# Optimization experiments

Measured on AMD Instinct MI355X. Metric: run time of the kernel, lower is better.

## Reference

```python
import jax, jax.numpy as jnp
import numpy as np

B, L_IMG, L_TXT, DM, H, D = 1, 4096, 512, 3072, 24, 128
EPS = 1e-6


def _rms(x, scale):
    # flax nnx RMSNorm: x * rsqrt(mean(x^2) + eps) * scale
    var = jnp.mean(jnp.square(x), axis=-1, keepdims=True)
    return x * jax.lax.rsqrt(var + EPS) * scale


def _qkv(x, W, qn, kn):
    b, l = x.shape[:2]
    qkv = (x @ W).reshape(b, l, 3, H, D).transpose(2, 0, 3, 1, 4)  # [3,B,H,L,D]
    q, k, v = qkv[0], qkv[1], qkv[2]
    return _rms(q, qn), _rms(k, kn), v


def setup_inputs() -> dict:
    key = jax.random.key(0)
    ks = jax.random.split(key, 8)
    s = 0.02
    return {
        "hidden_states": jax.random.normal(ks[0], (B, L_IMG, DM), jnp.float32),
        "encoder_hidden_states": jax.random.normal(ks[1], (B, L_TXT, DM), jnp.float32),
        "image_rotary_emb": jax.random.normal(ks[2], (L_TXT + L_IMG, D // 2, 4), jnp.float32),
        "W_iqkv": jax.random.normal(ks[3], (DM, 3 * H * D), jnp.float32) * s,
        "W_eqkv": jax.random.normal(ks[4], (DM, 3 * H * D), jnp.float32) * s,
        "W_iproj": jax.random.normal(ks[5], (H * D, DM), jnp.float32) * s,
        "b_iproj": jnp.zeros((DM,), jnp.float32),
        "W_eproj": jax.random.normal(ks[6], (H * D, DM), jnp.float32) * s,
        "b_eproj": jnp.zeros((DM,), jnp.float32),
        "qn_scale": jnp.ones((D,), jnp.float32),
        "kn_scale": jnp.ones((D,), jnp.float32),
        "eqn_scale": jnp.ones((D,), jnp.float32),
        "ekn_scale": jnp.ones((D,), jnp.float32),
    }


def reference(hidden_states, encoder_hidden_states, image_rotary_emb,
              W_iqkv, W_eqkv, W_iproj, b_iproj, W_eproj, b_eproj,
              qn_scale, kn_scale, eqn_scale, ekn_scale):
    scale = D ** -0.5
    l_txt = encoder_hidden_states.shape[1]

    q, k, v = _qkv(hidden_states, W_iqkv, qn_scale, kn_scale)           # [B,H,L_img,D]
    eq, ek, ev = _qkv(encoder_hidden_states, W_eqkv, eqn_scale, ekn_scale)

    q = jnp.concatenate((eq, q), axis=2)   # [B,H,L,D], L = L_txt + L_img
    k = jnp.concatenate((ek, k), axis=2)
    v = jnp.concatenate((ev, v), axis=2)

    # RoPE: freqs_cis [L, D/2, 2, 2]
    fc = image_rotary_emb.reshape(image_rotary_emb.shape[0], image_rotary_emb.shape[1], 2, 2)

    def rope(x):
        x_ = x.reshape(*x.shape[:-1], -1, 1, 2)  # [B,H,L,D/2,1,2]
        out = fc[..., 0] * x_[..., 0] + fc[..., 1] * x_[..., 1]  # [B,H,L,D/2,2]
        return out.reshape(*x.shape).astype(x.dtype)

    q, k = rope(q), rope(k)

    # flatten heads into feature dim BEFORE attention (faithful to original)
    def merge(x):
        b, h, l, d = x.shape
        return x.transpose(0, 2, 1, 3).reshape(b, l, h * d)

    qm, km, vm = merge(q), merge(k), merge(v)  # [B,L,H*D]

    attn = jax.nn.softmax(jnp.einsum('bqd,bkd->bqk', qm, km) * scale, axis=-1)
    out = jnp.einsum('bqk,bkd->bqd', attn, vm)  # [B,L,H*D]

    ctx_out, img_out = out[:, :l_txt], out[:, l_txt:]
    img_out = img_out @ W_iproj + b_iproj
    ctx_out = ctx_out @ W_eproj + b_eproj
    return img_out, ctx_out
```

## Files before the change

kernel.cpp:

```cpp
#include <hip/hip_runtime.h>
#include <hip/hip_bf16.h>
#include <cstdint>

typedef __attribute__((ext_vector_type(8))) short u16x8;
typedef _Float16 f16_t;
typedef __attribute__((ext_vector_type(8))) f16_t f16x8;
typedef __attribute__((ext_vector_type(4))) float f32x4;

#define L_TOT 4608
#define L_TXT 512
#define L_IMG 4096
#define NH 24
#define HD 128
#define DMODEL 3072
#define NQKV 9216
#define LOG2E 1.44269504088896340736f
#define S_SHIFT 32.0f

__device__ __forceinline__ ushort f2h(float f) {
  union { f16_t h; ushort u; } c; c.h = (f16_t)f; return c.u;
}
__device__ __forceinline__ float h2f(ushort u) {
  union { ushort u; f16_t h; } c; c.u = u; return (float)c.h;
}
__device__ __forceinline__ void gload16(const ushort* g, ushort* l) {
  __builtin_amdgcn_global_load_lds((const __attribute__((address_space(1))) void*)g,
                                   (__attribute__((address_space(3))) void*)l, 16, 0, 0);
}

__global__ void cvt_f32_f16(const float* __restrict__ src, ushort* __restrict__ dst,
                            int n8) {
  const int i = blockIdx.x * 256 + threadIdx.x;
  if (i >= n8) return;
  const f32x4 a = *(const f32x4*)(src + (size_t)i * 8);
  const f32x4 b = *(const f32x4*)(src + (size_t)i * 8 + 4);
  alignas(16) ushort o[8];
#pragma unroll
  for (int j = 0; j < 4; ++j) { o[j] = f2h(a[j]); o[4 + j] = f2h(b[j]); }
  *(u16x8*)(dst + (size_t)i * 8) = *(const u16x8*)o;
}

__global__ void tconv_w(const float* __restrict__ src, int C, int c0,
                        ushort* __restrict__ dst) {
  __shared__ ushort tile[64][72];
  const int nb = blockIdx.x << 6, kb = blockIdx.y << 6;
  const int t = threadIdx.x;
  const int lr = t >> 2, lc = (t & 3) << 4;
  const float* sp = src + (size_t)(kb + lr) * C + c0 + nb + lc;
  const f32x4 v0 = *(const f32x4*)sp;
  const f32x4 v1 = *(const f32x4*)(sp + 4);
  const f32x4 v2 = *(const f32x4*)(sp + 8);
  const f32x4 v3 = *(const f32x4*)(sp + 12);
#pragma unroll
  for (int i = 0; i < 4; ++i) {
    tile[lr][lc + i]      = f2h(v0[i]);
    tile[lr][lc + 4 + i]  = f2h(v1[i]);
    tile[lr][lc + 8 + i]  = f2h(v2[i]);
    tile[lr][lc + 12 + i] = f2h(v3[i]);
  }
  __syncthreads();
  const int cl = t & 63, rb = (t >> 6) << 4;
  alignas(16) ushort o[16];
#pragma unroll
  for (int i = 0; i < 16; ++i) o[i] = tile[rb + i][cl];
  ushort* dp = dst + (size_t)(nb + cl) * DMODEL + kb + rb;
  *(u16x8*)dp       = *(const u16x8*)o;
  *(u16x8*)(dp + 8) = *(const u16x8*)(o + 8);
}

__global__ void tconv_h(const ushort* __restrict__ src, ushort* __restrict__ dst,
                        int R, int C) {
  __shared__ ushort tile[64][72];
  const int r0 = blockIdx.y << 6, c0 = blockIdx.x << 6;
  const int t = threadIdx.x;
  const int lr = t >> 2, lc = (t & 3) << 4;
  const ushort* sp = src + (size_t)(r0 + lr) * C + c0 + lc;
  const u16x8 v0 = *(const u16x8*)sp;
  const u16x8 v1 = *(const u16x8*)(sp + 8);
#pragma unroll
  for (int i = 0; i < 8; ++i) {
    tile[lr][lc + i]     = ((const ushort*)&v0)[i];
    tile[lr][lc + 8 + i] = ((const ushort*)&v1)[i];
  }
  __syncthreads();
  const int cl = t & 63, rb = (t >> 6) << 4;
  alignas(16) ushort o[16];
#pragma unroll
  for (int i = 0; i < 16; ++i) o[i] = tile[rb + i][cl];
  ushort* dp = dst + (size_t)(c0 + cl) * R + r0 + rb;
  *(u16x8*)dp       = *(const u16x8*)o;
  *(u16x8*)(dp + 8) = *(const u16x8*)(o + 8);
}

template <int MODE>
__global__ __launch_bounds__(512, 2) void gemm256(
    const ushort* __restrict__ A, int lda, const ushort* __restrict__ Bt, int ldb,
    int M, int N, int K, void* __restrict__ out0, ushort* __restrict__ out1,
    ushort* __restrict__ out2, const float* __restrict__ bias, int l_off, int n_base) {
  __shared__ __align__(16) ushort lds[2][2][2][8192];
  int lin = blockIdx.y * gridDim.x + blockIdx.x;
  {
    const int nwg = gridDim.x * gridDim.y;
    const int q8 = nwg >> 3, r8 = nwg & 7;
    const int xcd = lin & 7, idx = lin >> 3;
    lin = (xcd < r8 ? xcd * (q8 + 1) : r8 * (q8 + 1) + (xcd - r8) * q8) + idx;
  }
  const int m0 = (lin % gridDim.x) << 8, n0 = (lin / gridDim.x) << 8;
  const int tid = threadIdx.x, w = tid >> 6, lane = tid & 63;
  const int wm = w >> 2, wn = w & 3;
  const int lr = lane & 15, g4 = lane >> 4;
  const int srow = lane >> 2;
  const int soff = 8 * ((lane & 3) ^ ((lane >> 3) & 3));
  f32x4 acc[8][4];
#pragma unroll
  for (int a = 0; a < 8; ++a)
#pragma unroll
    for (int b = 0; b < 4; ++b) acc[a][b] = (f32x4){0.f, 0.f, 0.f, 0.f};
  const int nt = K >> 6;

  auto stageA = [&](int h, int kt, int b) {
#pragma unroll
    for (int i = 0; i < 2; ++i) {
      const int j = w * 2 + i;
      gload16(A + (size_t)(m0 + 16 * j + srow) * lda + (kt << 6) + 32 * h + soff,
              &lds[b][h][0][j * 512]);
    }
  };
  auto stageB = [&](int h, int kt, int b) {
#pragma unroll
    for (int i = 0; i < 2; ++i) {
      const int j = w * 2 + i;
      gload16(Bt + (size_t)(n0 + 16 * j + srow) * ldb + (kt << 6) + 32 * h + soff,
              &lds[b][h][1][j * 512]);
    }
  };
  auto readA = [&](int h, int mi, int b) -> f16x8 {
    const int row = wm * 128 + mi * 16 + lr;
    const int byte = row * 64 + ((g4 ^ ((row >> 1) & 3)) << 4);
    return *(const f16x8*)((const char*)&lds[b][h][0][0] + byte);
  };
  auto readB = [&](int h, int ni, int b) -> f16x8 {
    const int row = wn * 64 + ni * 16 + lr;
    const int byte = row * 64 + ((g4 ^ ((row >> 1) & 3)) << 4);
    return *(const f16x8*)((const char*)&lds[b][h][1][0] + byte);
  };

  stageA(0, 0, 0); stageB(0, 0, 0); stageA(1, 0, 0); stageB(1, 0, 0);
  asm volatile("s_waitcnt vmcnt(4)" ::: "memory");
  asm volatile("s_barrier" ::: "memory");

  for (int kt = 0; kt < nt; ++kt) {
    const int c = kt & 1, sb = c ^ 1;
    const int st = (kt + 1 < nt) ? kt + 1 : 0;
    f16x8 bf[4], af[4];
#pragma unroll
    for (int ni = 0; ni < 4; ++ni) bf[ni] = readB(0, ni, c);
#pragma unroll
    for (int m = 0; m < 4; ++m) af[m] = readA(0, m, c);
    stageA(0, st, sb);
    asm volatile("s_barrier" ::: "memory");
    asm volatile("s_waitcnt lgkmcnt(0)" ::: "memory");
    __builtin_amdgcn_sched_barrier(0);
    __builtin_amdgcn_s_setprio(1);
#pragma unroll
    for (int m = 0; m < 4; ++m)
#pragma unroll
      for (int ni = 0; ni < 4; ++ni)
        acc[m][ni] = __builtin_amdgcn_mfma_f32_16x16x32_f16(af[m], bf[ni], acc[m][ni], 0, 0, 0);
    __builtin_amdgcn_s_setprio(0);
    asm volatile("s_barrier" ::: "memory");
#pragma unroll
    for (int m = 0; m < 4; ++m) af[m] = readA(0, 4 + m, c);
    stageB(0, st, sb);
    asm volatile("s_barrier" ::: "memory");
    asm volatile("s_waitcnt lgkmcnt(0)" ::: "memory");
    __builtin_amdgcn_sched_barrier(0);
    __builtin_amdgcn_s_setprio(1);
#pragma unroll
    for (int m = 0; m < 4; ++m)
#pragma unroll
      for (int ni = 0; ni < 4; ++ni)
        acc[4 + m][ni] = __builtin_amdgcn_mfma_f32_16x16x32_f16(af[m], bf[ni], acc[4 + m][ni], 0, 0, 0);
    __builtin_amdgcn_s_setprio(0);
    asm volatile("s_barrier" ::: "memory");
    asm volatile("s_waitcnt vmcnt(4)" ::: "memory");
    asm volatile("s_barrier" ::: "memory");
#pragma unroll
    for (int ni = 0; ni < 4; ++ni) bf[ni] = readB(1, ni, c);
#pragma unroll
    for (int m = 0; m < 4; ++m) af[m] = readA(1, m, c);
    stageA(1, st, sb);
    asm volatile("s_barrier" ::: "memory");
    asm volatile("s_waitcnt lgkmcnt(0)" ::: "memory");
    __builtin_amdgcn_sched_barrier(0);
    __builtin_amdgcn_s_setprio(1);
#pragma unroll
    for (int m = 0; m < 4; ++m)
#pragma unroll
      for (int ni = 0; ni < 4; ++ni)
        acc[m][ni] = __builtin_amdgcn_mfma_f32_16x16x32_f16(af[m], bf[ni], acc[m][ni], 0, 0, 0);
    __builtin_amdgcn_s_setprio(0);
    asm volatile("s_barrier" ::: "memory");
#pragma unroll
    for (int m = 0; m < 4; ++m) af[m] = readA(1, 4 + m, c);
    stageB(1, st, sb);
    asm volatile("s_barrier" ::: "memory");
    asm volatile("s_waitcnt lgkmcnt(0)" ::: "memory");
    __builtin_amdgcn_sched_barrier(0);
    __builtin_amdgcn_s_setprio(1);
#pragma unroll
    for (int m = 0; m < 4; ++m)
#pragma unroll
      for (int ni = 0; ni < 4; ++ni)
        acc[4 + m][ni] = __builtin_amdgcn_mfma_f32_16x16x32_f16(af[m], bf[ni], acc[4 + m][ni], 0, 0, 0);
    __builtin_amdgcn_s_setprio(0);
    asm volatile("s_waitcnt vmcnt(4)" ::: "memory");
    asm volatile("s_barrier" ::: "memory");
  }

  const int rb = (lane >> 4) << 2;
  const int cl = lane & 15;
  if (MODE == 0) {
    const int g = n_base + n0;
    const int which = g / DMODEL;
    const int col0 = g - which * DMODEL;
    ushort* dst = (which == 0) ? (ushort*)out0 : (which == 1) ? out1 : out2;
#pragma unroll
    for (int mi = 0; mi < 8; ++mi)
#pragma unroll
      for (int j = 0; j < 4; ++j) {
        const int l = l_off + m0 + wm * 128 + mi * 16 + rb + j;
        const size_t rbase = (size_t)l * DMODEL + col0 + wn * 64 + cl;
#pragma unroll
        for (int ni = 0; ni < 4; ++ni) dst[rbase + ni * 16] = f2h(acc[mi][ni][j]);
      }
  } else if (MODE == 1) {
    float* outf = (float*)out0;
    float bv[4];
#pragma unroll
    for (int ni = 0; ni < 4; ++ni) bv[ni] = bias[n0 + wn * 64 + ni * 16 + cl];
#pragma unroll
    for (int mi = 0; mi < 8; ++mi)
#pragma unroll
      for (int j = 0; j < 4; ++j) {
        const int r = m0 + wm * 128 + mi * 16 + rb + j;
        const size_t rbase = (size_t)r * N + n0 + wn * 64 + cl;
#pragma unroll
        for (int ni = 0; ni < 4; ++ni) outf[rbase + ni * 16] = acc[mi][ni][j] + bv[ni];
      }
  } else {
    ushort* outb = (ushort*)out0;
    const float sh = (MODE == 3) ? S_SHIFT : 0.0f;
#pragma unroll
    for (int mi = 0; mi < 8; ++mi)
#pragma unroll
      for (int j = 0; j < 4; ++j) {
        const int r = m0 + wm * 128 + mi * 16 + rb + j;
        const size_t rbase = (size_t)r * N + n0 + wn * 64 + cl;
#pragma unroll
        for (int ni = 0; ni < 4; ++ni) outb[rbase + ni * 16] = f2h(acc[mi][ni][j] - sh);
      }
  }
}

template <int MODE>
__global__ void gemm128(const ushort* __restrict__ A, int lda,
                        const ushort* __restrict__ Bt, int ldb,
                        int M, int N, int K, void* __restrict__ out0,
                        ushort* __restrict__ out1, ushort* __restrict__ out2,
                        const float* __restrict__ bias, int l_off, int n_base) {
  __shared__ __align__(16) ushort Alds[128 * 32];
  __shared__ __align__(16) ushort Blds[128 * 32];
  const int m0 = blockIdx.x << 7, n0 = blockIdx.y << 7;
  const int tid = threadIdx.x, wave = tid >> 6, lane = tid & 63;
  const int wr = wave >> 1, wc = wave & 1;
  const int lrow = lane & 15, lk8 = (lane >> 4) << 3;
  f32x4 acc[4][4];
#pragma unroll
  for (int a = 0; a < 4; ++a)
#pragma unroll
    for (int b = 0; b < 4; ++b) acc[a][b] = (f32x4){0.f, 0.f, 0.f, 0.f};
  const int nk = K >> 5;
  const ushort* Ap = A + (size_t)(m0 + (tid >> 2)) * lda + ((tid & 3) << 3);
  const ushort* Bp = Bt + (size_t)(n0 + (tid >> 2)) * ldb + ((tid & 3) << 3);
  for (int ks = 0; ks < nk; ++ks) {
    __syncthreads();
    const ushort* a0 = Ap + (ks << 5);
    gload16(a0, &Alds[wave << 9]);
    gload16(a0 + (size_t)64 * lda, &Alds[2048 + (wave << 9)]);
    const ushort* b0 = Bp + (ks << 5);
    gload16(b0, &Blds[wave << 9]);
    gload16(b0 + (size_t)64 * ldb, &Blds[2048 + (wave << 9)]);
    __syncthreads();
    f16x8 af[4], bfr[4];
#pragma unroll
    for (int mt = 0; mt < 4; ++mt)
      af[mt] = *(const f16x8*)&Alds[((wr << 6) + (mt << 4) + lrow) * 32 + lk8];
#pragma unroll
    for (int nt = 0; nt < 4; ++nt)
      bfr[nt] = *(const f16x8*)&Blds[((wc << 6) + (nt << 4) + lrow) * 32 + lk8];
#pragma unroll
    for (int mt = 0; mt < 4; ++mt)
#pragma unroll
      for (int nt = 0; nt < 4; ++nt)
        acc[mt][nt] = __builtin_amdgcn_mfma_f32_16x16x32_f16(af[mt], bfr[nt], acc[mt][nt], 0, 0, 0);
  }
  const int rb = (lane >> 4) << 2;
  if (MODE == 0) {
    const int g = n_base + n0;
    const int which = g / DMODEL;
    const int col0 = g - which * DMODEL;
    ushort* dst = (which == 0) ? (ushort*)out0 : (which == 1) ? out1 : out2;
#pragma unroll
    for (int mt = 0; mt < 4; ++mt)
#pragma unroll
      for (int j = 0; j < 4; ++j) {
        const int l = l_off + m0 + (wr << 6) + (mt << 4) + rb + j;
        const size_t rbase = (size_t)l * DMODEL + col0 + (wc << 6) + lrow;
#pragma unroll
        for (int nt = 0; nt < 4; ++nt) dst[rbase + (nt << 4)] = f2h(acc[mt][nt][j]);
      }
  } else {
    float* outf = (float*)out0;
    float bv[4];
#pragma unroll
    for (int nt = 0; nt < 4; ++nt) bv[nt] = bias[n0 + (wc << 6) + (nt << 4) + lrow];
#pragma unroll
    for (int mt = 0; mt < 4; ++mt)
#pragma unroll
      for (int j = 0; j < 4; ++j) {
        const int r = m0 + (wr << 6) + (mt << 4) + rb + j;
        const size_t rbase = (size_t)r * N + n0 + (wc << 6) + lrow;
#pragma unroll
        for (int nt = 0; nt < 4; ++nt) outf[rbase + (nt << 4)] = acc[mt][nt][j] + bv[nt];
      }
  }
}

__global__ void norm_rope(ushort* __restrict__ Q, ushort* __restrict__ Kg,
                          const float* __restrict__ rope,
                          const float* __restrict__ qn, const float* __restrict__ kn,
                          const float* __restrict__ eqn, const float* __restrict__ ekn) {
  const int idx = (blockIdx.x << 2) + (threadIdx.x >> 6);
  const int lane = threadIdx.x & 63;
  const int h = idx % NH, l = idx / NH;
  const float* qsc = (l < L_TXT) ? eqn : qn;
  const float* ksc = (l < L_TXT) ? ekn : kn;
  const size_t base = (size_t)l * DMODEL + h * HD + (lane << 1);
  const f32x4 fcv = *(const f32x4*)(rope + ((size_t)l * 64 + lane) * 4);
  const float fa = fcv[0], fb = fcv[1], fc = fcv[2], fd = fcv[3];
  const float s0 = qsc[lane << 1], s1 = qsc[(lane << 1) + 1];
  const float t0 = ksc[lane << 1], t1 = ksc[(lane << 1) + 1];
  {
    const uint32_t qv = *(const uint32_t*)&Q[base];
    float x0 = h2f((ushort)(qv & 0xffff)), x1 = h2f((ushort)(qv >> 16));
    float ss = x0 * x0 + x1 * x1;
#pragma unroll
    for (int m = 1; m < 64; m <<= 1) ss += __shfl_xor(ss, m);
    const float r = rsqrtf(ss * (1.0f / 128.0f) + 1e-6f);
    x0 *= r * s0;
    x1 *= r * s1;
    const float o0 = (fa * x0 + fb * x1) * 0.08838834764831845f;
    const float o1 = (fc * x0 + fd * x1) * 0.08838834764831845f;
    *(uint32_t*)&Q[base] = (uint32_t)f2h(o0) | ((uint32_t)f2h(o1) << 16);
  }
  {
    const uint32_t kv = *(const uint32_t*)&Kg[base];
    float x0 = h2f((ushort)(kv & 0xffff)), x1 = h2f((ushort)(kv >> 16));
    float ss = x0 * x0 + x1 * x1;
#pragma unroll
    for (int m = 1; m < 64; m <<= 1) ss += __shfl_xor(ss, m);
    const float r = rsqrtf(ss * (1.0f / 128.0f) + 1e-6f);
    x0 *= r * t0;
    x1 *= r * t1;
    const float o0 = fa * x0 + fb * x1;
    const float o1 = fc * x0 + fd * x1;
    *(uint32_t*)&Kg[base] = (uint32_t)f2h(o0) | ((uint32_t)f2h(o1) << 16);
  }
}

__global__ void softmax_rows(ushort* __restrict__ S) {
  const int r = blockIdx.x, tid = threadIdx.x;
  ushort* Sr = S + (size_t)r * L_TOT;
  float v[18];
  float m = -3.0e38f;
#pragma unroll
  for (int j = 0; j < 18; ++j) { v[j] = h2f(Sr[tid + (j << 8)]); m = fmaxf(m, v[j]); }
#pragma unroll
  for (int o = 1; o < 64; o <<= 1) m = fmaxf(m, __shfl_xor(m, o));
  __shared__ float redm[4], reds[4];
  const int wave = tid >> 6, lane = tid & 63;
  if (lane == 0) redm[wave] = m;
  __syncthreads();
  m = fmaxf(fmaxf(redm[0], redm[1]), fmaxf(redm[2], redm[3]));
  float s = 0.f;
#pragma unroll
  for (int j = 0; j < 18; ++j) { v[j] = exp2f((v[j] - m) * LOG2E); s += v[j]; }
#pragma unroll
  for (int o = 1; o < 64; o <<= 1) s += __shfl_xor(s, o);
  if (lane == 0) reds[wave] = s;
  __syncthreads();
  const float inv = 1.0f / (reds[0] + reds[1] + reds[2] + reds[3]);
#pragma unroll
  for (int j = 0; j < 18; ++j) Sr[tid + (j << 8)] = f2h(v[j] * inv);
}

extern "C" void kernel_launch(void* const* d_in, const int* in_sizes, int n_in,
                              void* d_out, int out_size, void* d_ws, size_t ws_size,
                              hipStream_t stream) {
  (void)in_sizes; (void)n_in; (void)out_size; (void)ws_size;
  const float* hidden  = (const float*)d_in[0];
  const float* enc     = (const float*)d_in[1];
  const float* rope    = (const float*)d_in[2];
  const float* W_iqkv  = (const float*)d_in[3];
  const float* W_eqkv  = (const float*)d_in[4];
  const float* W_iproj = (const float*)d_in[5];
  const float* b_iproj = (const float*)d_in[6];
  const float* W_eproj = (const float*)d_in[7];
  const float* b_eproj = (const float*)d_in[8];
  const float* qn  = (const float*)d_in[9];
  const float* kn  = (const float*)d_in[10];
  const float* eqn = (const float*)d_in[11];
  const float* ekn = (const float*)d_in[12];
  float* out = (float*)d_out;

  const size_t SZ_S  = (size_t)L_TOT * L_TOT;
  const size_t SZ_LD = (size_t)L_TOT * DMODEL;
  ushort* R0  = (ushort*)d_ws;
  ushort* CF  = R0;
  ushort* S   = R0;
  ushort* QR  = R0 + SZ_S;
  ushort* KR  = QR + SZ_LD;
  ushort* VR  = KR + SZ_LD;
  ushort* VT  = KR;
  ushort* AO  = QR;
  ushort* WP  = VR;
  ushort* WTD = (ushort*)out;

  dim3 blk(256);
  cvt_f32_f16<<<dim3(L_TXT * DMODEL / 8 / 256), blk, 0, stream>>>(enc, CF,
                                                                  L_TXT * DMODEL / 8);
  cvt_f32_f16<<<dim3(L_IMG * DMODEL / 8 / 256), blk, 0, stream>>>(
      hidden, CF + (size_t)L_TXT * DMODEL, L_IMG * DMODEL / 8);
  tconv_w<<<dim3(NQKV / 64, DMODEL / 64), blk, 0, stream>>>(W_iqkv, NQKV, 0, WTD);
  gemm256<0><<<dim3(L_IMG / 256, NQKV / 256), dim3(512), 0, stream>>>(
      CF + (size_t)L_TXT * DMODEL, DMODEL, WTD, DMODEL, L_IMG, NQKV, DMODEL,
      QR, KR, VR, nullptr, L_TXT, 0);
  tconv_w<<<dim3(NQKV / 64, DMODEL / 64), blk, 0, stream>>>(W_eqkv, NQKV, 0, WTD);
  gemm128<0><<<dim3(L_TXT / 128, NQKV / 128), blk, 0, stream>>>(
      CF, DMODEL, WTD, DMODEL, L_TXT, NQKV, DMODEL, QR, KR, VR, nullptr, 0, 0);
  norm_rope<<<dim3(L_TOT * NH / 4), blk, 0, stream>>>(QR, KR, rope, qn, kn, eqn, ekn);
  gemm256<3><<<dim3(L_TOT / 256, L_TOT / 256), dim3(512), 0, stream>>>(
      QR, DMODEL, KR, DMODEL, L_TOT, L_TOT, DMODEL, S, nullptr, nullptr, nullptr, 0, 0);
  softmax_rows<<<dim3(L_TOT), blk, 0, stream>>>(S);
  tconv_h<<<dim3(48, 72), blk, 0, stream>>>(VR, VT, L_TOT, DMODEL);
  gemm256<2><<<dim3(L_TOT / 256, DMODEL / 256), dim3(512), 0, stream>>>(
      S, L_TOT, VT, L_TOT, L_TOT, DMODEL, L_TOT, AO, nullptr, nullptr, nullptr, 0, 0);
  tconv_w<<<dim3(48, 48), blk, 0, stream>>>(W_iproj, DMODEL, 0, WP);
  gemm256<1><<<dim3(L_IMG / 256, DMODEL / 256), dim3(512), 0, stream>>>(
      AO + (size_t)L_TXT * DMODEL, DMODEL, WP, DMODEL, L_IMG, DMODEL, DMODEL,
      out, nullptr, nullptr, b_iproj, 0, 0);
  tconv_w<<<dim3(48, 48), blk, 0, stream>>>(W_eproj, DMODEL, 0, WP);
  gemm128<1><<<dim3(L_TXT / 128, DMODEL / 128), blk, 0, stream>>>(
      AO, DMODEL, WP, DMODEL, L_TXT, DMODEL, DMODEL,
      out + (size_t)L_IMG * DMODEL, nullptr, nullptr, b_eproj, 0, 0);
}
```

Baseline: 945.0 us.

## Restructure GEMM main loop into two half-K phases with fewer barriers

Reorganizes the double-buffered GEMM k-loop. Each half-K step now issues both the A and B prefetch for the next tile up front, loads all eight A fragments, and runs one 32-MFMA cluster. Before, each half-K step was split into two 16-MFMA sub-phases with a separate staging call and extra barriers. This cuts s_barrier and waitcnt points per iteration and lets longer MFMA runs hide the global-to-LDS copies. In exchange, eight A fragments are live at once, which raises VGPR pressure, and the wait/barrier placement is moved to the top of each phase.

```diff
diff --git a/kernel.cpp b/kernel.cpp
--- a/kernel.cpp
+++ b/kernel.cpp
@@ -146,76 +146,43 @@
   };
 
   stageA(0, 0, 0); stageB(0, 0, 0); stageA(1, 0, 0); stageB(1, 0, 0);
-  asm volatile("s_waitcnt vmcnt(4)" ::: "memory");
-  asm volatile("s_barrier" ::: "memory");
 
   for (int kt = 0; kt < nt; ++kt) {
     const int c = kt & 1, sb = c ^ 1;
     const int st = (kt + 1 < nt) ? kt + 1 : 0;
-    f16x8 bf[4], af[4];
+    f16x8 bf[4], af[8];
+    asm volatile("s_waitcnt vmcnt(4)" ::: "memory");
+    asm volatile("s_barrier" ::: "memory");
+    stageA(0, st, sb); stageB(0, st, sb);
 #pragma unroll
     for (int ni = 0; ni < 4; ++ni) bf[ni] = readB(0, ni, c);
 #pragma unroll
-    for (int m = 0; m < 4; ++m) af[m] = readA(0, m, c);
-    stageA(0, st, sb);
-    asm volatile("s_barrier" ::: "memory");
+    for (int m = 0; m < 8; ++m) af[m] = readA(0, m, c);
     asm volatile("s_waitcnt lgkmcnt(0)" ::: "memory");
     __builtin_amdgcn_sched_barrier(0);
     __builtin_amdgcn_s_setprio(1);
 #pragma unroll
-    for (int m = 0; m < 4; ++m)
+    for (int m = 0; m < 8; ++m)
 #pragma unroll
       for (int ni = 0; ni < 4; ++ni)
         acc[m][ni] = __builtin_amdgcn_mfma_f32_16x16x32_f16(af[m], bf[ni], acc[m][ni], 0, 0, 0);
     __builtin_amdgcn_s_setprio(0);
+    asm volatile("s_waitcnt vmcnt(4)" ::: "memory");
     asm volatile("s_barrier" ::: "memory");
-#pragma unroll
-    for (int m = 0; m < 4; ++m) af[m] = readA(0, 4 + m, c);
-    stageB(0, st, sb);
-    asm volatile("s_barrier" ::: "memory");
+    stageA(1, st, sb); stageB(1, st, sb);
+#pragma unroll
+    for (int ni = 0; ni < 4; ++ni) bf[ni] = readB(1, ni, c);
+#pragma unroll
+    for (int m = 0; m < 8; ++m) af[m] = readA(1, m, c);
     asm volatile("s_waitcnt lgkmcnt(0)" ::: "memory");
     __builtin_amdgcn_sched_barrier(0);
     __builtin_amdgcn_s_setprio(1);
 #pragma unroll
-    for (int m = 0; m < 4; ++m)
-#pragma unroll
-      for (int ni = 0; ni < 4; ++ni)
-        acc[4 + m][ni] = __builtin_amdgcn_mfma_f32_16x16x32_f16(af[m], bf[ni], acc[4 + m][ni], 0, 0, 0);
-    __builtin_amdgcn_s_setprio(0);
-    asm volatile("s_barrier" ::: "memory");
-    asm volatile("s_waitcnt vmcnt(4)" ::: "memory");
-    asm volatile("s_barrier" ::: "memory");
-#pragma unroll
-    for (int ni = 0; ni < 4; ++ni) bf[ni] = readB(1, ni, c);
-#pragma unroll
-    for (int m = 0; m < 4; ++m) af[m] = readA(1, m, c);
-    stageA(1, st, sb);
-    asm volatile("s_barrier" ::: "memory");
-    asm volatile("s_waitcnt lgkmcnt(0)" ::: "memory");
-    __builtin_amdgcn_sched_barrier(0);
-    __builtin_amdgcn_s_setprio(1);
-#pragma unroll
-    for (int m = 0; m < 4; ++m)
+    for (int m = 0; m < 8; ++m)
 #pragma unroll
       for (int ni = 0; ni < 4; ++ni)
         acc[m][ni] = __builtin_amdgcn_mfma_f32_16x16x32_f16(af[m], bf[ni], acc[m][ni], 0, 0, 0);
     __builtin_amdgcn_s_setprio(0);
-    asm volatile("s_barrier" ::: "memory");
-#pragma unroll
-    for (int m = 0; m < 4; ++m) af[m] = readA(1, 4 + m, c);
-    stageB(1, st, sb);
-    asm volatile("s_barrier" ::: "memory");
-    asm volatile("s_waitcnt lgkmcnt(0)" ::: "memory");
-    __builtin_amdgcn_sched_barrier(0);
-    __builtin_amdgcn_s_setprio(1);
-#pragma unroll
-    for (int m = 0; m < 4; ++m)
-#pragma unroll
-      for (int ni = 0; ni < 4; ++ni)
-        acc[4 + m][ni] = __builtin_amdgcn_mfma_f32_16x16x32_f16(af[m], bf[ni], acc[4 + m][ni], 0, 0, 0);
-    __builtin_amdgcn_s_setprio(0);
-    asm volatile("s_waitcnt vmcnt(4)" ::: "memory");
-    asm volatile("s_barrier" ::: "memory");
   }
 
   const int rb = (lane >> 4) << 2;
```

Result: no change. 939.7 us (-0.6%).
